# Optimization experiments

Hardware: AMD Instinct MI355X
Metric: run time of the kernel (lower is better)

Reference implementation:

```python
import jax, jax.numpy as jnp
import numpy as np

B, NB, BS, F = 4, 16, 256, 1024   # batch, num_blocks, block_size, features
H, D = 16, 64                     # heads, head_dim
ROPE = 32                         # rope_rotary_dims


def rotate_every_two(x):
    x1 = x[..., ::2]
    x2 = x[..., 1::2]
    return jnp.stack([-x2, x1], axis=-1).reshape(x.shape)


def apply_rope(x, num_blocks, block_size):
    # x: [B, NB, BS, H, rope_dim]
    rope_dim = x.shape[-1]
    inv_freq = 1.0 / 10000.0 ** (jnp.arange(0, rope_dim, 2, dtype=jnp.float32) / rope_dim)
    pos = jnp.arange(num_blocks * block_size, dtype=jnp.float32)
    ang = pos[:, None] * inv_freq[None, :]                       # [S, rope_dim/2]
    sin = jnp.sin(ang).reshape(num_blocks, block_size, rope_dim // 2)
    cos = jnp.cos(ang).reshape(num_blocks, block_size, rope_dim // 2)
    sin = jnp.repeat(sin[None, :, :, None, :], 2, axis=-1)       # [1, NB, BS, 1, rope_dim]
    cos = jnp.repeat(cos[None, :, :, None, :], 2, axis=-1)
    return x * cos + rotate_every_two(x) * sin


def setup_inputs() -> dict:
    key = jax.random.key(0)
    ks = jax.random.split(key, 8)
    s_in = 1.0 / np.sqrt(F)
    s_out = 1.0 / np.sqrt(H * D)
    return {
        "inputs_q": jax.random.normal(ks[0], (B, NB, BS, F), jnp.float32),
        "inputs_kv": jax.random.normal(ks[1], (B, NB, BS, F), jnp.float32),
        "Wq": jax.random.normal(ks[2], (F, H, D), jnp.float32) * s_in,
        "bq": jnp.zeros((H, D), jnp.float32),
        "Wk": jax.random.normal(ks[3], (F, H, D), jnp.float32) * s_in,
        "bk": jnp.zeros((H, D), jnp.float32),
        "Wv": jax.random.normal(ks[4], (F, H, D), jnp.float32) * s_in,
        "bv": jnp.zeros((H, D), jnp.float32),
        "Wo": jax.random.normal(ks[5], (H, D, F), jnp.float32) * s_out,
        "bo": jnp.zeros((F,), jnp.float32),
    }


def reference(inputs_q, inputs_kv, Wq, bq, Wk, bk, Wv, bv, Wo, bo):
    # QKV projections: [B, NB, BS, F] x [F, H, D] -> [B, NB, BS, H, D]
    q = jnp.einsum("bnsf,fhd->bnshd", inputs_q, Wq) + bq
    k = jnp.einsum("bnsf,fhd->bnshd", inputs_kv, Wk) + bk
    v = jnp.einsum("bnsf,fhd->bnshd", inputs_kv, Wv) + bv

    # RoPE on first ROPE dims of head_dim (intended semantics per docstring)
    q_rot, q_pass = q[..., :ROPE], q[..., ROPE:]
    k_rot, k_pass = k[..., :ROPE], k[..., ROPE:]
    q = jnp.concatenate([apply_rope(q_rot, NB, BS), q_pass], axis=-1)
    k = jnp.concatenate([apply_rope(k_rot, NB, BS), k_pass], axis=-1)

    # block-local dot-product attention (flax nn.dot_product_attention semantics)
    q = q / jnp.sqrt(jnp.asarray(D, q.dtype))
    scores = jnp.einsum("bnqhd,bnkhd->bnhqk", q, k)              # [B, NB, H, BS, BS]
    weights = jax.nn.softmax(scores, axis=-1)
    x = jnp.einsum("bnhqk,bnkhd->bnqhd", weights, v)             # [B, NB, BS, H, D]

    # output projection over (heads, head_dim)
    out = jnp.einsum("bnqhd,hdf->bnqf", x, Wo) + bo              # [B, NB, BS, F]
    return out
```

## Files before the change

### kernel.cpp

```cpp
#include <hip/hip_runtime.h>

typedef __attribute__((ext_vector_type(4))) float f32x4;
typedef __attribute__((ext_vector_type(8))) short s16x8;
typedef __attribute__((ext_vector_type(4))) unsigned short u16x4;

struct F2 { float c, s; };

__device__ __forceinline__ unsigned short f2b(float f) {
  unsigned u = __builtin_bit_cast(unsigned, f);
  u += 0x7FFFu + ((u >> 16) & 1u);
  return (unsigned short)(u >> 16);
}
__device__ __forceinline__ void gll16(const void* g, void* l) {
  __builtin_amdgcn_global_load_lds(
      (const __attribute__((address_space(1))) unsigned int*)g,
      (__attribute__((address_space(3))) unsigned int*)l, 16, 0, 0);
}
__device__ __forceinline__ f32x4 mfma16(s16x8 a, s16x8 b, f32x4 c) {
  return __builtin_amdgcn_mfma_f32_16x16x32_bf16(a, b, c, 0, 0, 0);
}

__global__ void k_cvt(const float* __restrict__ src, unsigned short* __restrict__ dst, int n4) {
  int i = blockIdx.x * 256 + threadIdx.x;
  int stride = gridDim.x * 256;
  for (; i < n4; i += stride) {
    f32x4 v = ((const f32x4*)src)[i];
    u16x4 o;
    o.x = f2b(v.x); o.y = f2b(v.y); o.z = f2b(v.z); o.w = f2b(v.w);
    ((u16x4*)dst)[i] = o;
  }
}

__global__ void k_sincos(F2* __restrict__ tab) {
  int idx = blockIdx.x * 256 + threadIdx.x;
  int pos = idx >> 4, fi = idx & 15;
  double inv = exp((double)fi * (-9.210340371976184 / 16.0));
  double a = (double)pos * inv;
  F2 r; r.c = (float)cos(a); r.s = (float)sin(a);
  tab[idx] = r;
}

__global__ void k_transpose(const float* __restrict__ wq,
                            const float* __restrict__ wk,
                            const float* __restrict__ wv,
                            const float* __restrict__ wo,
                            unsigned short* __restrict__ wtqkv,
                            unsigned short* __restrict__ wto) {
  __shared__ unsigned short tile[32][33];
  int z = blockIdx.z;
  const float* src = (z == 0) ? wq : (z == 1) ? wk : (z == 2) ? wv : wo;
  unsigned short* dst = (z < 3) ? (wtqkv + (size_t)z * 1048576) : wto;
  int bx = blockIdx.x * 32, by = blockIdx.y * 32;
  tile[threadIdx.y][threadIdx.x] = f2b(src[(size_t)(by + threadIdx.y) * 1024 + bx + threadIdx.x]);
  __syncthreads();
  dst[(size_t)(bx + threadIdx.y) * 1024 + by + threadIdx.x] = tile[threadIdx.x][threadIdx.y];
}

__global__ __launch_bounds__(256, 2) void k_qkv(
    const unsigned short* __restrict__ Xq,
    const unsigned short* __restrict__ Xkv,
    const unsigned short* __restrict__ WT,
    const float* __restrict__ bq,
    const float* __restrict__ bk,
    const float* __restrict__ bv,
    const F2* __restrict__ tab,
    unsigned short* __restrict__ qbuf,
    unsigned short* __restrict__ kbuf,
    unsigned short* __restrict__ vbuf) {
  __shared__ __align__(16) unsigned short Al[128 * 64];
  __shared__ __align__(16) unsigned short Bl[128 * 64];
  int bid = blockIdx.x;
  int swz = (bid & 7) * 384 + (bid >> 3);
  int mt = swz / 24, nt = swz % 24;
  int m0 = mt * 128, n0 = nt * 128;
  int which = n0 >> 10;
  const unsigned short* X = (which == 0) ? Xq : Xkv;
  const float* bias = (which == 0) ? bq : (which == 1) ? bk : bv;
  unsigned short* dst = (which == 0) ? qbuf : (which == 1) ? kbuf : vbuf;
  int n0l = n0 & 1023;
  int tid = threadIdx.x, wid = tid >> 6, lane = tid & 63;
  int fr = lane & 15, fg = lane >> 4;
  int wr = (wid >> 1) * 64, wc = (wid & 1) * 64;
  int sr = lane >> 3, sc8 = (lane & 7) * 8;

  f32x4 acc[4][4] = {};
  for (int kt = 0; kt < 16; ++kt) {
    int kb = kt * 64;
#pragma unroll
    for (int tt = 0; tt < 4; ++tt) {
      int t = wid * 4 + tt;
      gll16(X  + (size_t)(m0 + t * 8 + sr) * 1024 + kb + sc8, &Al[t * 512]);
      gll16(WT + (size_t)(n0 + t * 8 + sr) * 1024 + kb + sc8, &Bl[t * 512]);
    }
    __syncthreads();
#pragma unroll
    for (int ks = 0; ks < 2; ++ks) {
      int ko = ks * 32 + fg * 8;
      s16x8 af[4], bfr[4];
#pragma unroll
      for (int i = 0; i < 4; ++i) af[i]  = *(const s16x8*)&Al[(wr + i * 16 + fr) * 64 + ko];
#pragma unroll
      for (int i = 0; i < 4; ++i) bfr[i] = *(const s16x8*)&Bl[(wc + i * 16 + fr) * 64 + ko];
#pragma unroll
      for (int mi = 0; mi < 4; ++mi)
#pragma unroll
        for (int ni = 0; ni < 4; ++ni)
          acc[mi][ni] = mfma16(af[mi], bfr[ni], acc[mi][ni]);
    }
    __syncthreads();
  }
#pragma unroll
  for (int mi = 0; mi < 4; ++mi)
#pragma unroll
    for (int ni = 0; ni < 4; ++ni) {
      int c = wc + ni * 16 + fr;
      int col = n0l + c;
      int h = col >> 6, d = col & 63;
      float bz = bias[col];
      bool rope = (which < 2) && (d < 32);
#pragma unroll
      for (int j = 0; j < 4; ++j) {
        int mg = m0 + wr + mi * 16 + fg * 4 + j;
        float v = acc[mi][ni][j] + bz;
        if (rope) {
          float p = __shfl_xor(v, 1);
          F2 cs = tab[(mg & 4095) * 16 + (d >> 1)];
          v = (d & 1) ? fmaf(v, cs.c, p * cs.s) : fmaf(v, cs.c, -(p * cs.s));
        }
        if (which == 0) v *= 0.125f;
        int bn = mg >> 8, s2 = mg & 255;
        dst[((size_t)(bn * 16 + h) * 256 + s2) * 64 + d] = f2b(v);
      }
    }
}

__global__ __launch_bounds__(256, 1) void k_attn(
    const unsigned short* __restrict__ qbuf,
    const unsigned short* __restrict__ kbuf,
    const unsigned short* __restrict__ vbuf,
    unsigned short* __restrict__ xbuf) {
  __shared__ __align__(16) unsigned short Kl[256 * 64];
  __shared__ __align__(16) unsigned short Vt[64 * 264];
  __shared__ __align__(16) unsigned short Pl[4][16 * 264];
  int g = blockIdx.x;
  size_t base = (size_t)g * (256 * 64);
  const unsigned short* Q = qbuf + base;
  const unsigned short* K = kbuf + base;
  const unsigned short* V = vbuf + base;
  int bn = g >> 4, h = g & 15;
  int tid = threadIdx.x, wid = tid >> 6, lane = tid & 63;
  int fr = lane & 15, fg = lane >> 4;

#pragma unroll
  for (int tt = 0; tt < 8; ++tt) {
    int t = wid * 8 + tt;
    int r = t * 8 + (lane >> 3);
    int cp = lane & 7;
    int csrc = cp ^ (r & 7);
    gll16(K + r * 64 + csrc * 8, &Kl[t * 512]);
  }
#pragma unroll
  for (int c8 = 0; c8 < 8; ++c8) {
    s16x8 vv = *(const s16x8*)&V[tid * 64 + c8 * 8];
#pragma unroll
    for (int j = 0; j < 8; ++j)
      Vt[(c8 * 8 + j) * 264 + tid] = (unsigned short)vv[j];
  }
  __syncthreads();

  unsigned short* P = Pl[wid];
  int f7 = fr & 7;
  int c0 = (fg ^ f7) * 8;
  int c1 = ((4 + fg) ^ f7) * 8;
  for (int mtile = 0; mtile < 4; ++mtile) {
    int q0 = wid * 64 + mtile * 16;
    s16x8 qa0 = *(const s16x8*)&Q[(q0 + fr) * 64 + fg * 8];
    s16x8 qa1 = *(const s16x8*)&Q[(q0 + fr) * 64 + 32 + fg * 8];
    f32x4 sc[16] = {};
#pragma unroll
    for (int nt = 0; nt < 16; ++nt) {
      int rr = nt * 16 + fr;
      s16x8 kb0 = *(const s16x8*)&Kl[rr * 64 + c0];
      sc[nt] = mfma16(qa0, kb0, sc[nt]);
      s16x8 kb1 = *(const s16x8*)&Kl[rr * 64 + c1];
      sc[nt] = mfma16(qa1, kb1, sc[nt]);
    }
    float rs[4];
#pragma unroll
    for (int j = 0; j < 4; ++j) {
      float m = sc[0][j];
#pragma unroll
      for (int nt = 1; nt < 16; ++nt) m = fmaxf(m, sc[nt][j]);
      m = fmaxf(m, __shfl_xor(m, 1));
      m = fmaxf(m, __shfl_xor(m, 2));
      m = fmaxf(m, __shfl_xor(m, 4));
      m = fmaxf(m, __shfl_xor(m, 8));
      float sum = 0.f;
#pragma unroll
      for (int nt = 0; nt < 16; ++nt) {
        float p = __expf(sc[nt][j] - m);
        sum += p;
        P[(fg * 4 + j) * 264 + nt * 16 + fr] = f2b(p);
      }
      sum += __shfl_xor(sum, 1);
      sum += __shfl_xor(sum, 2);
      sum += __shfl_xor(sum, 4);
      sum += __shfl_xor(sum, 8);
      rs[j] = 1.0f / sum;
    }
    f32x4 o[4] = {};
#pragma unroll
    for (int ks = 0; ks < 8; ++ks) {
      s16x8 pa = *(const s16x8*)&P[fr * 264 + ks * 32 + fg * 8];
#pragma unroll
      for (int nt = 0; nt < 4; ++nt) {
        s16x8 vb = *(const s16x8*)&Vt[(nt * 16 + fr) * 264 + ks * 32 + fg * 8];
        o[nt] = mfma16(pa, vb, o[nt]);
      }
    }
#pragma unroll
    for (int nt = 0; nt < 4; ++nt)
#pragma unroll
      for (int j = 0; j < 4; ++j) {
        int srow = q0 + fg * 4 + j;
        int d = nt * 16 + fr;
        xbuf[((size_t)(bn * 256 + srow)) * 1024 + h * 64 + d] = f2b(o[nt][j] * rs[j]);
      }
  }
}

__global__ __launch_bounds__(256, 2) void k_out(
    const unsigned short* __restrict__ Xb,
    const unsigned short* __restrict__ WT,
    const float* __restrict__ bo,
    float* __restrict__ out) {
  __shared__ __align__(16) unsigned short Al[128 * 64];
  __shared__ __align__(16) unsigned short Bl[128 * 64];
  int bid = blockIdx.x;
  int swz = (bid & 7) * 128 + (bid >> 3);
  int mt = swz >> 3, nt = swz & 7;
  int m0 = mt * 128, n0 = nt * 128;
  int tid = threadIdx.x, wid = tid >> 6, lane = tid & 63;
  int fr = lane & 15, fg = lane >> 4;
  int wr = (wid >> 1) * 64, wc = (wid & 1) * 64;
  int sr = lane >> 3, sc8 = (lane & 7) * 8;
  f32x4 acc[4][4] = {};
  for (int kt = 0; kt < 16; ++kt) {
    int kb = kt * 64;
#pragma unroll
    for (int tt = 0; tt < 4; ++tt) {
      int t = wid * 4 + tt;
      gll16(Xb + (size_t)(m0 + t * 8 + sr) * 1024 + kb + sc8, &Al[t * 512]);
      gll16(WT + (size_t)(n0 + t * 8 + sr) * 1024 + kb + sc8, &Bl[t * 512]);
    }
    __syncthreads();
#pragma unroll
    for (int ks = 0; ks < 2; ++ks) {
      int ko = ks * 32 + fg * 8;
      s16x8 af[4], bfr[4];
#pragma unroll
      for (int i = 0; i < 4; ++i) af[i]  = *(const s16x8*)&Al[(wr + i * 16 + fr) * 64 + ko];
#pragma unroll
      for (int i = 0; i < 4; ++i) bfr[i] = *(const s16x8*)&Bl[(wc + i * 16 + fr) * 64 + ko];
#pragma unroll
      for (int mi = 0; mi < 4; ++mi)
#pragma unroll
        for (int ni = 0; ni < 4; ++ni)
          acc[mi][ni] = mfma16(af[mi], bfr[ni], acc[mi][ni]);
    }
    __syncthreads();
  }
#pragma unroll
  for (int mi = 0; mi < 4; ++mi)
#pragma unroll
    for (int ni = 0; ni < 4; ++ni) {
      int c = wc + ni * 16 + fr;
      float bz = bo[n0 + c];
#pragma unroll
      for (int j = 0; j < 4; ++j) {
        int mg = m0 + wr + mi * 16 + fg * 4 + j;
        out[(size_t)mg * 1024 + n0 + c] = acc[mi][ni][j] + bz;
      }
    }
}

extern "C" void kernel_launch(void* const* d_in, const int* in_sizes, int n_in,
                              void* d_out, int out_size, void* d_ws, size_t ws_size,
                              hipStream_t stream) {
  const float* Xq  = (const float*)d_in[0];
  const float* Xkv = (const float*)d_in[1];
  const float* Wq  = (const float*)d_in[2];
  const float* bq  = (const float*)d_in[3];
  const float* Wk  = (const float*)d_in[4];
  const float* bk  = (const float*)d_in[5];
  const float* Wv  = (const float*)d_in[6];
  const float* bv  = (const float*)d_in[7];
  const float* Wo  = (const float*)d_in[8];
  const float* bo  = (const float*)d_in[9];
  float* out = (float*)d_out;

  char* ws = (char*)d_ws;
  size_t off = 0;
  F2* tab = (F2*)(ws + off);                           off += (size_t)65536 * sizeof(F2);
  unsigned short* WTqkv = (unsigned short*)(ws + off); off += (size_t)3 * 1048576 * 2;
  unsigned short* WTo   = (unsigned short*)(ws + off); off += (size_t)1048576 * 2;
  unsigned short* Xqb   = (unsigned short*)(ws + off); off += (size_t)16777216 * 2;
  unsigned short* Xkvb  = (unsigned short*)(ws + off); off += (size_t)16777216 * 2;
  unsigned short* qb = (unsigned short*)(ws + off); off += (size_t)16777216 * 2;
  unsigned short* kb = (unsigned short*)(ws + off); off += (size_t)16777216 * 2;
  unsigned short* vb = (unsigned short*)(ws + off); off += (size_t)16777216 * 2;
  unsigned short* xb = Xqb;

  k_cvt<<<2048, 256, 0, stream>>>(Xq,  Xqb,  4194304);
  k_cvt<<<2048, 256, 0, stream>>>(Xkv, Xkvb, 4194304);
  k_sincos<<<256, 256, 0, stream>>>(tab);
  k_transpose<<<dim3(32, 32, 4), dim3(32, 32), 0, stream>>>(Wq, Wk, Wv, Wo, WTqkv, WTo);
  k_qkv<<<3072, 256, 0, stream>>>(Xqb, Xkvb, WTqkv, bq, bk, bv, tab, qb, kb, vb);
  k_attn<<<1024, 256, 0, stream>>>(qb, kb, vb, xb);
  k_out<<<1024, 256, 0, stream>>>(xb, WTo, bo, out);
}
```

Measured before the change: 290.0 us.

## Swizzle GEMM LDS tiles, stage epilogues through LDS, widen attention blocks, fuse prep kernels

The two separate input-conversion launches and the sin/cos table launch become a single prep kernel. Both GEMMs now use an XOR-swizzled LDS layout so fragment reads avoid bank conflicts. Their epilogues write results into LDS first and then issue coalesced 16-byte global stores instead of scattered 2- and 4-byte stores. The attention kernel moves to 512 threads (8 waves) per block, so each wave handles 32 query rows. The LDS staging in the epilogues adds extra shared-memory traffic, and the larger attention block allocates more LDS for P.

New measurement: 259.2 us. 1.12x faster.

```diff
diff --git a/kernel.cpp b/kernel.cpp
--- a/kernel.cpp
+++ b/kernel.cpp
@@ -20,24 +20,28 @@
   return __builtin_amdgcn_mfma_f32_16x16x32_bf16(a, b, c, 0, 0, 0);
 }
 
-__global__ void k_cvt(const float* __restrict__ src, unsigned short* __restrict__ dst, int n4) {
-  int i = blockIdx.x * 256 + threadIdx.x;
-  int stride = gridDim.x * 256;
-  for (; i < n4; i += stride) {
-    f32x4 v = ((const f32x4*)src)[i];
-    u16x4 o;
-    o.x = f2b(v.x); o.y = f2b(v.y); o.z = f2b(v.z); o.w = f2b(v.w);
-    ((u16x4*)dst)[i] = o;
-  }
-}
-
-__global__ void k_sincos(F2* __restrict__ tab) {
-  int idx = blockIdx.x * 256 + threadIdx.x;
-  int pos = idx >> 4, fi = idx & 15;
-  double inv = exp((double)fi * (-9.210340371976184 / 16.0));
-  double a = (double)pos * inv;
-  F2 r; r.c = (float)cos(a); r.s = (float)sin(a);
-  tab[idx] = r;
+__global__ void k_prep(const float* __restrict__ Xq, const float* __restrict__ Xkv,
+                       unsigned short* __restrict__ Xqb, unsigned short* __restrict__ Xkvb,
+                       F2* __restrict__ tab) {
+  int b = blockIdx.x;
+  if (b < 4096) {
+    const float* src = (b < 2048) ? Xq : Xkv;
+    unsigned short* dst = (b < 2048) ? Xqb : Xkvb;
+    int i = (b & 2047) * 256 + threadIdx.x;
+    for (; i < 4194304; i += 2048 * 256) {
+      f32x4 v = ((const f32x4*)src)[i];
+      u16x4 o;
+      o.x = f2b(v.x); o.y = f2b(v.y); o.z = f2b(v.z); o.w = f2b(v.w);
+      ((u16x4*)dst)[i] = o;
+    }
+  } else {
+    int idx = (b - 4096) * 256 + threadIdx.x;
+    int pos = idx >> 4, fi = idx & 15;
+    double inv = exp((double)fi * (-9.210340371976184 / 16.0));
+    double a = (double)pos * inv;
+    F2 r; r.c = (float)cos(a); r.s = (float)sin(a);
+    tab[idx] = r;
+  }
 }
 
 __global__ void k_transpose(const float* __restrict__ wq,
@@ -67,8 +71,9 @@
     unsigned short* __restrict__ qbuf,
     unsigned short* __restrict__ kbuf,
     unsigned short* __restrict__ vbuf) {
-  __shared__ __align__(16) unsigned short Al[128 * 64];
-  __shared__ __align__(16) unsigned short Bl[128 * 64];
+  __shared__ __align__(16) unsigned short S[16384];
+  unsigned short* Al = S;
+  unsigned short* Bl = S + 8192;
   int bid = blockIdx.x;
   int swz = (bid & 7) * 384 + (bid >> 3);
   int mt = swz / 24, nt = swz % 24;
@@ -79,9 +84,10 @@
   unsigned short* dst = (which == 0) ? qbuf : (which == 1) ? kbuf : vbuf;
   int n0l = n0 & 1023;
   int tid = threadIdx.x, wid = tid >> 6, lane = tid & 63;
-  int fr = lane & 15, fg = lane >> 4;
+  int fr = lane & 15, fg = lane >> 4, f7 = fr & 7;
   int wr = (wid >> 1) * 64, wc = (wid & 1) * 64;
-  int sr = lane >> 3, sc8 = (lane & 7) * 8;
+  int sr = lane >> 3, scp = lane & 7;
+  int g0 = (fg ^ f7) * 8, g1 = ((4 + fg) ^ f7) * 8;
 
   f32x4 acc[4][4] = {};
   for (int kt = 0; kt < 16; ++kt) {
@@ -89,18 +95,20 @@
 #pragma unroll
     for (int tt = 0; tt < 4; ++tt) {
       int t = wid * 4 + tt;
-      gll16(X  + (size_t)(m0 + t * 8 + sr) * 1024 + kb + sc8, &Al[t * 512]);
-      gll16(WT + (size_t)(n0 + t * 8 + sr) * 1024 + kb + sc8, &Bl[t * 512]);
+      int row = t * 8 + sr;
+      int cs = (scp ^ (row & 7)) * 8;
+      gll16(X  + (size_t)(m0 + row) * 1024 + kb + cs, &Al[t * 512]);
+      gll16(WT + (size_t)(n0 + row) * 1024 + kb + cs, &Bl[t * 512]);
     }
     __syncthreads();
 #pragma unroll
     for (int ks = 0; ks < 2; ++ks) {
-      int ko = ks * 32 + fg * 8;
+      int gk = ks ? g1 : g0;
       s16x8 af[4], bfr[4];
 #pragma unroll
-      for (int i = 0; i < 4; ++i) af[i]  = *(const s16x8*)&Al[(wr + i * 16 + fr) * 64 + ko];
-#pragma unroll
-      for (int i = 0; i < 4; ++i) bfr[i] = *(const s16x8*)&Bl[(wc + i * 16 + fr) * 64 + ko];
+      for (int i = 0; i < 4; ++i) af[i]  = *(const s16x8*)&Al[(wr + i * 16 + fr) * 64 + gk];
+#pragma unroll
+      for (int i = 0; i < 4; ++i) bfr[i] = *(const s16x8*)&Bl[(wc + i * 16 + fr) * 64 + gk];
 #pragma unroll
       for (int mi = 0; mi < 4; ++mi)
 #pragma unroll
@@ -109,62 +117,79 @@
     }
     __syncthreads();
   }
-#pragma unroll
-  for (int mi = 0; mi < 4; ++mi)
-#pragma unroll
-    for (int ni = 0; ni < 4; ++ni) {
-      int c = wc + ni * 16 + fr;
-      int col = n0l + c;
-      int h = col >> 6, d = col & 63;
-      float bz = bias[col];
-      bool rope = (which < 2) && (d < 32);
+
+  unsigned short* W = S + wid * 4096;
+  int hh = (n0l + wc) >> 6;
+  int rbase = m0 + wr;
+  int bn = rbase >> 8;
+#pragma unroll
+  for (int nf = 0; nf < 4; ++nf) {
+    int d = nf * 16 + fr;
+    int col = n0l + wc + d;
+    float bz = bias[col];
+    bool rope = (which < 2) && (nf < 2);
+#pragma unroll
+    for (int mf = 0; mf < 4; ++mf) {
 #pragma unroll
       for (int j = 0; j < 4; ++j) {
-        int mg = m0 + wr + mi * 16 + fg * 4 + j;
-        float v = acc[mi][ni][j] + bz;
+        int row = mf * 16 + fg * 4 + j;
+        int mg = rbase + row;
+        float v = acc[mf][nf][j] + bz;
         if (rope) {
           float p = __shfl_xor(v, 1);
           F2 cs = tab[(mg & 4095) * 16 + (d >> 1)];
           v = (d & 1) ? fmaf(v, cs.c, p * cs.s) : fmaf(v, cs.c, -(p * cs.s));
         }
         if (which == 0) v *= 0.125f;
-        int bn = mg >> 8, s2 = mg & 255;
-        dst[((size_t)(bn * 16 + h) * 256 + s2) * 64 + d] = f2b(v);
-      }
-    }
-}
-
-__global__ __launch_bounds__(256, 1) void k_attn(
+        W[row * 64 + (((d >> 3) ^ (row & 7)) << 3) + (d & 7)] = f2b(v);
+      }
+    }
+  }
+  asm volatile("s_waitcnt lgkmcnt(0)" ::: "memory");
+  __builtin_amdgcn_sched_barrier(0);
+  size_t gbase = ((size_t)(bn * 16 + hh) * 256 + (rbase & 255)) * 64;
+#pragma unroll
+  for (int it = 0; it < 8; ++it) {
+    int r = it * 8 + (lane >> 3);
+    int ch = (lane & 7) ^ (r & 7);
+    s16x8 vv = *(const s16x8*)&W[r * 64 + ch * 8];
+    *(s16x8*)&dst[gbase + r * 64 + (lane & 7) * 8] = vv;
+  }
+}
+
+__global__ __launch_bounds__(512, 1) void k_attn(
     const unsigned short* __restrict__ qbuf,
     const unsigned short* __restrict__ kbuf,
     const unsigned short* __restrict__ vbuf,
     unsigned short* __restrict__ xbuf) {
   __shared__ __align__(16) unsigned short Kl[256 * 64];
   __shared__ __align__(16) unsigned short Vt[64 * 264];
-  __shared__ __align__(16) unsigned short Pl[4][16 * 264];
-  int g = blockIdx.x;
-  size_t base = (size_t)g * (256 * 64);
+  __shared__ __align__(16) unsigned short Pl[8][16 * 264];
+  int gb = blockIdx.x;
+  size_t base = (size_t)gb * (256 * 64);
   const unsigned short* Q = qbuf + base;
   const unsigned short* K = kbuf + base;
   const unsigned short* V = vbuf + base;
-  int bn = g >> 4, h = g & 15;
+  int bn = gb >> 4, h = gb & 15;
   int tid = threadIdx.x, wid = tid >> 6, lane = tid & 63;
   int fr = lane & 15, fg = lane >> 4;
 
 #pragma unroll
-  for (int tt = 0; tt < 8; ++tt) {
-    int t = wid * 8 + tt;
+  for (int tt = 0; tt < 4; ++tt) {
+    int t = wid * 4 + tt;
     int r = t * 8 + (lane >> 3);
-    int cp = lane & 7;
-    int csrc = cp ^ (r & 7);
+    int csrc = (lane & 7) ^ (r & 7);
     gll16(K + r * 64 + csrc * 8, &Kl[t * 512]);
   }
-#pragma unroll
-  for (int c8 = 0; c8 < 8; ++c8) {
-    s16x8 vv = *(const s16x8*)&V[tid * 64 + c8 * 8];
-#pragma unroll
-    for (int j = 0; j < 8; ++j)
-      Vt[(c8 * 8 + j) * 264 + tid] = (unsigned short)vv[j];
+  {
+    int rv = tid >> 1, chalf = (tid & 1) * 32;
+#pragma unroll
+    for (int c8 = 0; c8 < 4; ++c8) {
+      s16x8 vv = *(const s16x8*)&V[rv * 64 + chalf + c8 * 8];
+#pragma unroll
+      for (int j = 0; j < 8; ++j)
+        Vt[(chalf + c8 * 8 + j) * 264 + rv] = (unsigned short)vv[j];
+    }
   }
   __syncthreads();
 
@@ -172,8 +197,8 @@
   int f7 = fr & 7;
   int c0 = (fg ^ f7) * 8;
   int c1 = ((4 + fg) ^ f7) * 8;
-  for (int mtile = 0; mtile < 4; ++mtile) {
-    int q0 = wid * 64 + mtile * 16;
+  for (int mtile = 0; mtile < 2; ++mtile) {
+    int q0 = wid * 32 + mtile * 16;
     s16x8 qa0 = *(const s16x8*)&Q[(q0 + fr) * 64 + fg * 8];
     s16x8 qa1 = *(const s16x8*)&Q[(q0 + fr) * 64 + 32 + fg * 8];
     f32x4 sc[16] = {};
@@ -234,34 +259,39 @@
     const unsigned short* __restrict__ WT,
     const float* __restrict__ bo,
     float* __restrict__ out) {
-  __shared__ __align__(16) unsigned short Al[128 * 64];
-  __shared__ __align__(16) unsigned short Bl[128 * 64];
+  __shared__ __align__(16) unsigned short S[16384];
+  unsigned short* Al = S;
+  unsigned short* Bl = S + 8192;
   int bid = blockIdx.x;
   int swz = (bid & 7) * 128 + (bid >> 3);
   int mt = swz >> 3, nt = swz & 7;
   int m0 = mt * 128, n0 = nt * 128;
   int tid = threadIdx.x, wid = tid >> 6, lane = tid & 63;
-  int fr = lane & 15, fg = lane >> 4;
+  int fr = lane & 15, fg = lane >> 4, f7 = fr & 7;
   int wr = (wid >> 1) * 64, wc = (wid & 1) * 64;
-  int sr = lane >> 3, sc8 = (lane & 7) * 8;
+  int sr = lane >> 3, scp = lane & 7;
+  int g0 = (fg ^ f7) * 8, g1 = ((4 + fg) ^ f7) * 8;
+
   f32x4 acc[4][4] = {};
   for (int kt = 0; kt < 16; ++kt) {
     int kb = kt * 64;
 #pragma unroll
     for (int tt = 0; tt < 4; ++tt) {
       int t = wid * 4 + tt;
-      gll16(Xb + (size_t)(m0 + t * 8 + sr) * 1024 + kb + sc8, &Al[t * 512]);
-      gll16(WT + (size_t)(n0 + t * 8 + sr) * 1024 + kb + sc8, &Bl[t * 512]);
+      int row = t * 8 + sr;
+      int cs = (scp ^ (row & 7)) * 8;
+      gll16(Xb + (size_t)(m0 + row) * 1024 + kb + cs, &Al[t * 512]);
+      gll16(WT + (size_t)(n0 + row) * 1024 + kb + cs, &Bl[t * 512]);
     }
     __syncthreads();
 #pragma unroll
     for (int ks = 0; ks < 2; ++ks) {
-      int ko = ks * 32 + fg * 8;
+      int gk = ks ? g1 : g0;
       s16x8 af[4], bfr[4];
 #pragma unroll
-      for (int i = 0; i < 4; ++i) af[i]  = *(const s16x8*)&Al[(wr + i * 16 + fr) * 64 + ko];
-#pragma unroll
-      for (int i = 0; i < 4; ++i) bfr[i] = *(const s16x8*)&Bl[(wc + i * 16 + fr) * 64 + ko];
+      for (int i = 0; i < 4; ++i) af[i]  = *(const s16x8*)&Al[(wr + i * 16 + fr) * 64 + gk];
+#pragma unroll
+      for (int i = 0; i < 4; ++i) bfr[i] = *(const s16x8*)&Bl[(wc + i * 16 + fr) * 64 + gk];
 #pragma unroll
       for (int mi = 0; mi < 4; ++mi)
 #pragma unroll
@@ -270,18 +300,39 @@
     }
     __syncthreads();
   }
-#pragma unroll
-  for (int mi = 0; mi < 4; ++mi)
-#pragma unroll
-    for (int ni = 0; ni < 4; ++ni) {
-      int c = wc + ni * 16 + fr;
-      float bz = bo[n0 + c];
-#pragma unroll
-      for (int j = 0; j < 4; ++j) {
-        int mg = m0 + wr + mi * 16 + fg * 4 + j;
-        out[(size_t)mg * 1024 + n0 + c] = acc[mi][ni][j] + bz;
-      }
-    }
+
+  float* Wf = (float*)S + wid * 2048;
+  int rbase = m0 + wr;
+#pragma unroll
+  for (int p = 0; p < 2; ++p) {
+#pragma unroll
+    for (int nf = 0; nf < 4; ++nf) {
+      int d = nf * 16 + fr;
+      float bz = bo[n0 + wc + d];
+#pragma unroll
+      for (int mh = 0; mh < 2; ++mh) {
+        int mf = p * 2 + mh;
+#pragma unroll
+        for (int j = 0; j < 4; ++j) {
+          int rloc = mh * 16 + fg * 4 + j;
+          Wf[rloc * 64 + (((d >> 3) ^ (rloc & 7)) << 3) + (d & 7)] = acc[mf][nf][j] + bz;
+        }
+      }
+    }
+    asm volatile("s_waitcnt lgkmcnt(0)" ::: "memory");
+    __builtin_amdgcn_sched_barrier(0);
+#pragma unroll
+    for (int it = 0; it < 8; ++it) {
+      int rloc = it * 4 + (lane >> 4);
+      int cpair = lane & 15;
+      int ch = (cpair >> 1) ^ (rloc & 7);
+      f32x4 vv = *(const f32x4*)&Wf[rloc * 64 + ch * 8 + (cpair & 1) * 4];
+      int mg = rbase + p * 32 + rloc;
+      *(f32x4*)&out[(size_t)mg * 1024 + n0 + wc + cpair * 4] = vv;
+    }
+    asm volatile("s_waitcnt lgkmcnt(0)" ::: "memory");
+    __builtin_amdgcn_sched_barrier(0);
+  }
 }
 
 extern "C" void kernel_launch(void* const* d_in, const int* in_sizes, int n_in,
@@ -311,11 +362,9 @@
   unsigned short* vb = (unsigned short*)(ws + off); off += (size_t)16777216 * 2;
   unsigned short* xb = Xqb;
 
-  k_cvt<<<2048, 256, 0, stream>>>(Xq,  Xqb,  4194304);
-  k_cvt<<<2048, 256, 0, stream>>>(Xkv, Xkvb, 4194304);
-  k_sincos<<<256, 256, 0, stream>>>(tab);
+  k_prep<<<4352, 256, 0, stream>>>(Xq, Xkv, Xqb, Xkvb, tab);
   k_transpose<<<dim3(32, 32, 4), dim3(32, 32), 0, stream>>>(Wq, Wk, Wv, Wo, WTqkv, WTo);
   k_qkv<<<3072, 256, 0, stream>>>(Xqb, Xkvb, WTqkv, bq, bk, bv, tab, qb, kb, vb);
-  k_attn<<<1024, 256, 0, stream>>>(qb, kb, vb, xb);
+  k_attn<<<1024, 512, 0, stream>>>(qb, kb, vb, xb);
   k_out<<<1024, 256, 0, stream>>>(xb, WTo, bo, out);
 }
```
